# Kernel tuning notes

Measured on AMD Instinct MI355X. Metric: run time of the kernel, lower is better.

Reference implementation:

```python
import jax, jax.numpy as jnp
import numpy as np

NUM_GROUPS = 50   # hardcoded in convert_groupandcate_to_one_hot
ALPHA = 2.0       # forward() default
MARGIN = 0.8      # forward() default


def setup_inputs() -> dict:
    key = jax.random.key(0)
    k1, k2, k3, k4 = jax.random.split(key, 4)
    B, C, N = 4, 64, 4096
    l0_points = jax.random.normal(k1, (B, N, 3), dtype=jnp.float32)
    Fsim = jax.random.normal(k2, (B, C, N), dtype=jnp.float32)
    target = jax.random.randint(k3, (B, N), 0, NUM_GROUPS, dtype=jnp.int32)
    # sprinkle some -1 (ungrouped) labels, matching real SGPN data
    drop = jax.random.uniform(k4, (B, N)) < 0.02
    target = jnp.where(drop, jnp.int32(-1), target)
    return {"l0_points": l0_points, "Fsim": Fsim, "target": target}


def reference(l0_points, Fsim, target):
    B, C, N = Fsim.shape
    # pairwise squared-distance Gram matrix: D[i,j] = |f_i|^2 + |f_j|^2 - 2<f_i,f_j>
    r = jnp.sum(Fsim * Fsim, axis=1)                      # [B, N]
    gram = jnp.einsum('bcn,bcm->bnm', Fsim, Fsim)          # [B, N, N]
    D = jnp.maximum(r[:, :, None] + r[:, None, :] - 2.0 * gram, 0.0)

    # one-hot group labels; label -1 contributes all-zeros row
    valid = (target != -1)
    one_hot = (jax.nn.one_hot(jnp.where(valid, target, 0), NUM_GROUPS,
                              dtype=jnp.float32)
               * valid[..., None].astype(jnp.float32))     # [B, N, G]

    same = jnp.einsum('bng,bmg->bnm', one_hot, one_hot)    # same-group indicator
    eye = jnp.eye(N, dtype=same.dtype)
    same = same * (1.0 - eye) + eye                        # diagonal forced to 1
    diff = 1.0 - same

    pos = same * D
    neg = ALPHA * diff * jnp.maximum(MARGIN - D, 0.0)

    # NOTE: original returns grouplabels (not the count weights) as group_mask,
    # so the weight is the outer product of the raw integer labels.
    tf = target.astype(jnp.float32)
    w = tf[:, :, None] * tf[:, None, :]                    # [B, N, N]

    return jnp.mean((pos + neg) * w)
```

## Files before the change

kernel.cpp:

```cpp
#include <hip/hip_runtime.h>
#include <hip/hip_bf16.h>
#include <stdint.h>


#define NT 32
#define TRI 528
#define NBLK (4*TRI)
#define SCALE (1.0f/67108864.0f)

typedef __attribute__((ext_vector_type(4))) float f32x4;
typedef __attribute__((ext_vector_type(8))) __bf16 bf16x8;

__device__ __forceinline__ void async_load16(const void* g, void* l) {
    __builtin_amdgcn_global_load_lds(
        (const __attribute__((address_space(1))) uint32_t*)g,
        (__attribute__((address_space(3))) uint32_t*)l,
        16, 0, 0);
}

__global__ __launch_bounds__(256) void sgpn_prep(
    const float* __restrict__ Fsim, const int* __restrict__ target,
    unsigned short* __restrict__ gA, float* __restrict__ gR,
    float* __restrict__ gK, float* __restrict__ gW)
{
    __shared__ float sPart[4][64];

    int blk = blockIdx.x;
    int b = blk >> 6;
    int n0 = (blk & 63) * 64;
    int lane = threadIdx.x & 63;
    int wave = threadIdx.x >> 6;

    int n = n0 + lane;
    int gp = b * 4096 + n;
    const float* src = Fsim + (size_t)b * 64 * 4096 + n;
    int tile = n >> 7, row = n & 127;
    unsigned short* dst = gA + (size_t)(b * NT + tile) * 8192 + row * 8;

    float racc = 0.f;
    #pragma unroll
    for (int q = 0; q < 2; ++q) {
        int chunk = wave * 2 + q;
        unsigned us[8];
        #pragma unroll
        for (int j = 0; j < 8; ++j) {
            float f = src[(size_t)(chunk * 8 + j) * 4096];
            unsigned u = __float_as_uint(f);
            u += 0x7fffu + ((u >> 16) & 1u);
            us[j] = u >> 16;
            float fb = __uint_as_float(us[j] << 16);
            racc = fmaf(fb, fb, racc);
        }
        uint4 pk;
        pk.x = us[0] | (us[1] << 16);
        pk.y = us[2] | (us[3] << 16);
        pk.z = us[4] | (us[5] << 16);
        pk.w = us[6] | (us[7] << 16);
        *(uint4*)(dst + chunk * 1024) = pk;
    }
    sPart[wave][lane] = racc;
    __syncthreads();
    if (wave == 0) {
        gR[gp] = (sPart[0][lane] + sPart[1][lane]) +
                 (sPart[2][lane] + sPart[3][lane]);
        int tg = target[gp];
        gK[gp] = (tg >= 0) ? (float)tg : -(float)(n + 2);
        gW[gp] = (float)tg;
    }
}

__global__ __launch_bounds__(256) void sgpn_main(
    const unsigned short* __restrict__ gA,
    const float* __restrict__ gR, const float* __restrict__ gK,
    const float* __restrict__ gW, float* __restrict__ gP)
{
    __shared__ __align__(16) unsigned short lA[8192];
    __shared__ __align__(16) unsigned short lB[8192];
    __shared__ __align__(16) float sRr[128], sKr[128], sWr[128];
    __shared__ __align__(16) float sRc[128], sKc[128], sWc[128];
    __shared__ float sRed[4];

    int bid = blockIdx.x;
    int b = bid / TRI;
    int t = bid - b * TRI;
    int tj = (int)((sqrtf(8.0f * (float)t + 1.0f) - 1.0f) * 0.5f);
    while ((tj + 1) * (tj + 2) / 2 <= t) ++tj;
    while (tj * (tj + 1) / 2 > t) --tj;
    int ti = t - tj * (tj + 1) / 2;

    int tid = threadIdx.x;

    const unsigned short* tileA = gA + (size_t)(b * NT + ti) * 8192;
    const unsigned short* tileB = gA + (size_t)(b * NT + tj) * 8192;
    #pragma unroll
    for (int it = 0; it < 4; ++it) {
        int e = it * 256 + tid;
        async_load16(tileA + e * 8, lA + e * 8);
        async_load16(tileB + e * 8, lB + e * 8);
    }
    {
        int half = tid >> 7;
        int p0 = tid & 127;
        int gp = b * 4096 + (half ? tj : ti) * 128 + p0;
        float rv = gR[gp], kv = gK[gp], wv = gW[gp];
        if (half == 0) { sRr[p0] = rv; sKr[p0] = kv; sWr[p0] = wv; }
        else           { sRc[p0] = rv; sKc[p0] = kv; sWc[p0] = wv; }
    }
    __syncthreads();

    int lane = tid & 63;
    int wave = tid >> 6;
    int wr = wave >> 1, wc = wave & 1;
    int quad = lane >> 4, lcol = lane & 15;

    f32x4 acc[4][4];
    #pragma unroll
    for (int i = 0; i < 4; ++i)
        #pragma unroll
        for (int j = 0; j < 4; ++j)
            acc[i][j] = (f32x4)0.f;

    #pragma unroll
    for (int kb = 0; kb < 2; ++kb) {
        int chunk = kb * 4 + quad;
        bf16x8 fa[4], fb[4];
        #pragma unroll
        for (int i = 0; i < 4; ++i)
            fa[i] = *(const bf16x8*)&lA[chunk * 1024 + (wr * 64 + i * 16 + lcol) * 8];
        #pragma unroll
        for (int j = 0; j < 4; ++j)
            fb[j] = *(const bf16x8*)&lB[chunk * 1024 + (wc * 64 + j * 16 + lcol) * 8];
        #pragma unroll
        for (int i = 0; i < 4; ++i)
            #pragma unroll
            for (int j = 0; j < 4; ++j)
                acc[i][j] = __builtin_amdgcn_mfma_f32_16x16x32_bf16(fa[i], fb[j], acc[i][j], 0, 0, 0);
    }

    float rcv[4], kcv[4], wcv[4];
    #pragma unroll
    for (int j = 0; j < 4; ++j) {
        int cl = wc * 64 + j * 16 + lcol;
        rcv[j] = sRc[cl]; kcv[j] = sKc[cl]; wcv[j] = sWc[cl];
    }

    float sum = 0.f;
    #pragma unroll
    for (int i = 0; i < 4; ++i) {
        int rb = wr * 64 + i * 16 + quad * 4;
        f32x4 rr4 = *(const f32x4*)&sRr[rb];
        f32x4 kr4 = *(const f32x4*)&sKr[rb];
        f32x4 wr4 = *(const f32x4*)&sWr[rb];
        #pragma unroll
        for (int r = 0; r < 4; ++r) {
            float rrow = rr4[r], krow = kr4[r], wrow = wr4[r];
            float psum = 0.f;
            #pragma unroll
            for (int j = 0; j < 4; ++j) {
                float g  = acc[i][j][r];
                float d0 = fmaf(-2.f, g, rrow + rcv[j]);
                float D  = fmaxf(d0, 0.f);
                float h  = fmaxf(fmaf(D, -2.f, 1.6f), 0.f);
                float v  = (krow == kcv[j]) ? D : h;
                psum = fmaf(v, wcv[j], psum);
            }
            sum = fmaf(psum, wrow, sum);
        }
    }

    #pragma unroll
    for (int off = 32; off > 0; off >>= 1)
        sum += __shfl_down(sum, off, 64);
    if (lane == 0) sRed[wave] = sum;
    __syncthreads();
    if (tid == 0) {
        float tot = (sRed[0] + sRed[1]) + (sRed[2] + sRed[3]);
        float mult = (ti == tj) ? 1.f : 2.f;
        gP[bid] = tot * mult;
    }
}

__global__ __launch_bounds__(256) void sgpn_reduce(
    const float* __restrict__ gP, float* __restrict__ out)
{
    __shared__ float sr[4];
    int tid = threadIdx.x;
    float s = 0.f;
    for (int i = tid; i < NBLK; i += 256) s += gP[i];
    #pragma unroll
    for (int off = 32; off > 0; off >>= 1)
        s += __shfl_down(s, off, 64);
    if ((tid & 63) == 0) sr[tid >> 6] = s;
    __syncthreads();
    if (tid == 0)
        out[0] = ((sr[0] + sr[1]) + (sr[2] + sr[3])) * SCALE;
}

extern "C" void kernel_launch(void* const* d_in, const int* in_sizes, int n_in,
                              void* d_out, int out_size, void* d_ws, size_t ws_size,
                              hipStream_t stream) {
    const float* Fsim  = (const float*)d_in[1];
    const int* target  = (const int*)d_in[2];
    float* out = (float*)d_out;

    char* ws = (char*)d_ws;
    unsigned short* gA = (unsigned short*)ws;
    float* gR = (float*)(ws + (2u << 20));
    float* gK = (float*)(ws + (2u << 20) + (64u << 10));
    float* gW = (float*)(ws + (2u << 20) + (128u << 10));
    float* gP = (float*)(ws + (2u << 20) + (192u << 10));

    sgpn_prep<<<256, 256, 0, stream>>>(Fsim, target, gA, gR, gK, gW);
    sgpn_main<<<NBLK, 256, 0, stream>>>(gA, gR, gK, gW, gP);
    sgpn_reduce<<<1, 256, 0, stream>>>(gP, out);
}
```

Baseline: 78.68 us.

## Make main kernel persistent with double-buffered async tile prefetch

Launches a fixed grid of 512 blocks instead of one block per tile pair. Each block walks 4-5 tile pairs and prefetches the next pair's bf16 tiles and per-point metadata into a second LDS buffer while computing the current one. The per-pair weight multiplier is folded into a running total, and the final reduce reads exactly two partials per thread. This trades launch and per-block setup overhead, plus exposed load latency, for doubled LDS use (about 70KB per block) and an uneven tail where some blocks handle one extra pair.

```diff
diff --git a/kernel.cpp b/kernel.cpp
--- a/kernel.cpp
+++ b/kernel.cpp
@@ -5,7 +5,8 @@
 
 #define NT 32
 #define TRI 528
-#define NBLK (4*TRI)
+#define NPAIR (4*TRI)
+#define NBLK 512
 #define SCALE (1.0f/67108864.0f)
 
 typedef __attribute__((ext_vector_type(4))) float f32x4;
@@ -69,115 +70,123 @@
     }
 }
 
-__global__ __launch_bounds__(256) void sgpn_main(
+__global__ __launch_bounds__(256, 2) void sgpn_main(
     const unsigned short* __restrict__ gA,
     const float* __restrict__ gR, const float* __restrict__ gK,
     const float* __restrict__ gW, float* __restrict__ gP)
 {
-    __shared__ __align__(16) unsigned short lA[8192];
-    __shared__ __align__(16) unsigned short lB[8192];
-    __shared__ __align__(16) float sRr[128], sKr[128], sWr[128];
-    __shared__ __align__(16) float sRc[128], sKc[128], sWc[128];
+    __shared__ __align__(16) unsigned short lT[2][2][8192];
+    __shared__ __align__(16) float sM[2][2][3][128];
     __shared__ float sRed[4];
-
-    int bid = blockIdx.x;
-    int b = bid / TRI;
-    int t = bid - b * TRI;
-    int tj = (int)((sqrtf(8.0f * (float)t + 1.0f) - 1.0f) * 0.5f);
-    while ((tj + 1) * (tj + 2) / 2 <= t) ++tj;
-    while (tj * (tj + 1) / 2 > t) --tj;
-    int ti = t - tj * (tj + 1) / 2;
+    __shared__ float sMult[2];
 
     int tid = threadIdx.x;
-
-    const unsigned short* tileA = gA + (size_t)(b * NT + ti) * 8192;
-    const unsigned short* tileB = gA + (size_t)(b * NT + tj) * 8192;
-    #pragma unroll
-    for (int it = 0; it < 4; ++it) {
-        int e = it * 256 + tid;
-        async_load16(tileA + e * 8, lA + e * 8);
-        async_load16(tileB + e * 8, lB + e * 8);
-    }
-    {
-        int half = tid >> 7;
-        int p0 = tid & 127;
-        int gp = b * 4096 + (half ? tj : ti) * 128 + p0;
-        float rv = gR[gp], kv = gK[gp], wv = gW[gp];
-        if (half == 0) { sRr[p0] = rv; sKr[p0] = kv; sWr[p0] = wv; }
-        else           { sRc[p0] = rv; sKc[p0] = kv; sWc[p0] = wv; }
-    }
-    __syncthreads();
-
     int lane = tid & 63;
     int wave = tid >> 6;
+    int g = blockIdx.x;
+    int np = (g < (NPAIR - 4 * NBLK)) ? 5 : 4;
+
+    auto stage = [&](int P, int buf) {
+        int b = P / TRI;
+        int t = P - b * TRI;
+        int tj = (int)((sqrtf(8.0f * (float)t + 1.0f) - 1.0f) * 0.5f);
+        while ((tj + 1) * (tj + 2) / 2 <= t) ++tj;
+        while (tj * (tj + 1) / 2 > t) --tj;
+        int ti = t - tj * (tj + 1) / 2;
+
+        const unsigned short* tA = gA + (size_t)(b * NT + ti) * 8192;
+        const unsigned short* tB = gA + (size_t)(b * NT + tj) * 8192;
+        #pragma unroll
+        for (int it = 0; it < 4; ++it) {
+            int e = it * 256 + tid;
+            async_load16(tA + e * 8, &lT[buf][0][e * 8]);
+            async_load16(tB + e * 8, &lT[buf][1][e * 8]);
+        }
+        int half = tid >> 7, p0 = tid & 127;
+        int gp = b * 4096 + (half ? tj : ti) * 128 + p0;
+        sM[buf][half][0][p0] = gR[gp];
+        sM[buf][half][1][p0] = gK[gp];
+        sM[buf][half][2][p0] = gW[gp];
+        if (tid == 0) sMult[buf] = (ti == tj) ? 1.f : 2.f;
+    };
+
     int wr = wave >> 1, wc = wave & 1;
     int quad = lane >> 4, lcol = lane & 15;
 
-    f32x4 acc[4][4];
-    #pragma unroll
-    for (int i = 0; i < 4; ++i)
-        #pragma unroll
-        for (int j = 0; j < 4; ++j)
-            acc[i][j] = (f32x4)0.f;
-
-    #pragma unroll
-    for (int kb = 0; kb < 2; ++kb) {
-        int chunk = kb * 4 + quad;
-        bf16x8 fa[4], fb[4];
+    float total = 0.f;
+    stage(g, 0);
+
+    for (int q = 0; q < np; ++q) {
+        __syncthreads();
+        int buf = q & 1;
+        if (q + 1 < np) stage(g + (q + 1) * NBLK, buf ^ 1);
+
+        f32x4 acc[4][4];
         #pragma unroll
         for (int i = 0; i < 4; ++i)
-            fa[i] = *(const bf16x8*)&lA[chunk * 1024 + (wr * 64 + i * 16 + lcol) * 8];
-        #pragma unroll
-        for (int j = 0; j < 4; ++j)
-            fb[j] = *(const bf16x8*)&lB[chunk * 1024 + (wc * 64 + j * 16 + lcol) * 8];
-        #pragma unroll
-        for (int i = 0; i < 4; ++i)
             #pragma unroll
             for (int j = 0; j < 4; ++j)
-                acc[i][j] = __builtin_amdgcn_mfma_f32_16x16x32_bf16(fa[i], fb[j], acc[i][j], 0, 0, 0);
-    }
-
-    float rcv[4], kcv[4], wcv[4];
-    #pragma unroll
-    for (int j = 0; j < 4; ++j) {
-        int cl = wc * 64 + j * 16 + lcol;
-        rcv[j] = sRc[cl]; kcv[j] = sKc[cl]; wcv[j] = sWc[cl];
-    }
-
-    float sum = 0.f;
-    #pragma unroll
-    for (int i = 0; i < 4; ++i) {
-        int rb = wr * 64 + i * 16 + quad * 4;
-        f32x4 rr4 = *(const f32x4*)&sRr[rb];
-        f32x4 kr4 = *(const f32x4*)&sKr[rb];
-        f32x4 wr4 = *(const f32x4*)&sWr[rb];
-        #pragma unroll
-        for (int r = 0; r < 4; ++r) {
-            float rrow = rr4[r], krow = kr4[r], wrow = wr4[r];
-            float psum = 0.f;
-            #pragma unroll
-            for (int j = 0; j < 4; ++j) {
-                float g  = acc[i][j][r];
-                float d0 = fmaf(-2.f, g, rrow + rcv[j]);
-                float D  = fmaxf(d0, 0.f);
-                float h  = fmaxf(fmaf(D, -2.f, 1.6f), 0.f);
-                float v  = (krow == kcv[j]) ? D : h;
-                psum = fmaf(v, wcv[j], psum);
+                acc[i][j] = (f32x4)0.f;
+
+        #pragma unroll
+        for (int kb = 0; kb < 2; ++kb) {
+            int chunk = kb * 4 + quad;
+            bf16x8 fa[4], fb[4];
+            #pragma unroll
+            for (int i = 0; i < 4; ++i)
+                fa[i] = *(const bf16x8*)&lT[buf][0][chunk * 1024 + (wr * 64 + i * 16 + lcol) * 8];
+            #pragma unroll
+            for (int j = 0; j < 4; ++j)
+                fb[j] = *(const bf16x8*)&lT[buf][1][chunk * 1024 + (wc * 64 + j * 16 + lcol) * 8];
+            #pragma unroll
+            for (int i = 0; i < 4; ++i)
+                #pragma unroll
+                for (int j = 0; j < 4; ++j)
+                    acc[i][j] = __builtin_amdgcn_mfma_f32_16x16x32_bf16(fa[i], fb[j], acc[i][j], 0, 0, 0);
+        }
+
+        float rcv[4], kcv[4], wcv[4];
+        #pragma unroll
+        for (int j = 0; j < 4; ++j) {
+            int cl = wc * 64 + j * 16 + lcol;
+            rcv[j] = sM[buf][1][0][cl];
+            kcv[j] = sM[buf][1][1][cl];
+            wcv[j] = sM[buf][1][2][cl];
+        }
+
+        float sum = 0.f;
+        #pragma unroll
+        for (int i = 0; i < 4; ++i) {
+            int rb = wr * 64 + i * 16 + quad * 4;
+            f32x4 rr4 = *(const f32x4*)&sM[buf][0][0][rb];
+            f32x4 kr4 = *(const f32x4*)&sM[buf][0][1][rb];
+            f32x4 wr4 = *(const f32x4*)&sM[buf][0][2][rb];
+            #pragma unroll
+            for (int r = 0; r < 4; ++r) {
+                float rrow = rr4[r], krow = kr4[r], wrow = wr4[r];
+                float psum = 0.f;
+                #pragma unroll
+                for (int j = 0; j < 4; ++j) {
+                    float gacc = acc[i][j][r];
+                    float d0 = fmaf(-2.f, gacc, rrow + rcv[j]);
+                    float D  = fmaxf(d0, 0.f);
+                    float h  = fmaxf(fmaf(D, -2.f, 1.6f), 0.f);
+                    float v  = (krow == kcv[j]) ? D : h;
+                    psum = fmaf(v, wcv[j], psum);
+                }
+                sum = fmaf(psum, wrow, sum);
             }
-            sum = fmaf(psum, wrow, sum);
-        }
+        }
+        total = fmaf(sum, sMult[buf], total);
     }
 
     #pragma unroll
     for (int off = 32; off > 0; off >>= 1)
-        sum += __shfl_down(sum, off, 64);
-    if (lane == 0) sRed[wave] = sum;
+        total += __shfl_down(total, off, 64);
+    if (lane == 0) sRed[wave] = total;
     __syncthreads();
-    if (tid == 0) {
-        float tot = (sRed[0] + sRed[1]) + (sRed[2] + sRed[3]);
-        float mult = (ti == tj) ? 1.f : 2.f;
-        gP[bid] = tot * mult;
-    }
+    if (tid == 0)
+        gP[g] = (sRed[0] + sRed[1]) + (sRed[2] + sRed[3]);
 }
 
 __global__ __launch_bounds__(256) void sgpn_reduce(
@@ -185,8 +194,7 @@
 {
     __shared__ float sr[4];
     int tid = threadIdx.x;
-    float s = 0.f;
-    for (int i = tid; i < NBLK; i += 256) s += gP[i];
+    float s = gP[tid] + gP[tid + 256];
     #pragma unroll
     for (int off = 32; off > 0; off >>= 1)
         s += __shfl_down(s, off, 64);
```

Measured after the change: 77.68 us. No clear change (-1.3%).
